# Kernel optimization log

Hardware: AMD Instinct MI355X
Metric: run time of the kernel (lower is better)

The kernel has to match this reference:

```python
import jax, jax.numpy as jnp
import numpy as np


def setup_inputs() -> dict:
    key = jax.random.key(0)
    ks = jax.random.split(key, 5)
    B, S, E, H = 2, 2048, 1024, 16
    scale = 1.0 / np.sqrt(E)
    return {
        "input": jax.random.normal(ks[0], (B, S, E), dtype=jnp.float32),
        "Wqkv": jax.random.normal(ks[1], (3 * E, E), dtype=jnp.float32) * scale,
        "bqkv": jax.random.normal(ks[2], (3 * E,), dtype=jnp.float32) * 0.01,
        "Wo": jax.random.normal(ks[3], (E, E), dtype=jnp.float32) * scale,
        "bo": jax.random.normal(ks[4], (E,), dtype=jnp.float32) * 0.01,
    }


def reference(input, Wqkv, bqkv, Wo, bo):
    H = 16
    B, S, E = input.shape
    dh = E // H
    # fused QKV projection: [B, S, 3E]
    qkv = input @ Wqkv.T + bqkv
    qkv = qkv.reshape(B, S, 3, H, dh)
    qkv = jnp.transpose(qkv, (2, 0, 3, 1, 4))  # [3, B, H, S, dh]
    q, k, v = qkv[0], qkv[1], qkv[2]
    # scores [B, H, Sq, Sk]
    scores = jnp.einsum("bhqd,bhkd->bhqk", q, k) / jnp.sqrt(jnp.float32(dh))
    # NOTE: original code softmaxes over dim=2 (the QUERY axis) — reproduced faithfully
    attn = jax.nn.softmax(scores, axis=2)
    out = jnp.einsum("bhqk,bhkd->bhqd", attn, v)  # [B, H, S, dh]
    out = jnp.transpose(out, (0, 2, 1, 3)).reshape(B, S, E)
    return out @ Wo.T + bo
```

## Files before the change

kernel.cpp:

```cpp
#include <hip/hip_runtime.h>
#include <math.h>

#define B_ 2
#define S_ 2048
#define E_ 1024
#define H_ 16
#define DH_ 64
#define NE3_ 3072
#define MTOT_ (B_*S_)
#define QSCALE_ 0.18033688011112042f

typedef __bf16 bf16;
typedef bf16 bf16x8 __attribute__((ext_vector_type(8)));
typedef bf16 bf16x4 __attribute__((ext_vector_type(4)));
typedef float f32x4 __attribute__((ext_vector_type(4)));
typedef float f32x16 __attribute__((ext_vector_type(16)));
typedef unsigned u32x2 __attribute__((ext_vector_type(2)));
typedef unsigned u32x4 __attribute__((ext_vector_type(4)));

#define MFMA16(a,b,c) __builtin_amdgcn_mfma_f32_16x16x32_bf16(a,b,c,0,0,0)
#define MFMA32(a,b,c) __builtin_amdgcn_mfma_f32_32x32x16_bf16(a,b,c,0,0,0)

#define F_(r) ((((r) & 7) ^ (((r) >> 3) & 7)))

__device__ inline void* lds_swz(void* base, int row, int bytecol) {
    return (char*)base + row * 128 + (bytecol ^ (F_(row) << 4));
}

__device__ inline unsigned cvt_pk_bf16(float lo, float hi) {
    unsigned r;
    asm("v_cvt_pk_bf16_f32 %0, %1, %2" : "=v"(r) : "v"(lo), "v"(hi));
    return r;
}

__device__ inline void permswap32(unsigned &x, unsigned &y) {
    u32x2 r = __builtin_amdgcn_permlane32_swap(x, y, false, false);
    x = r.x; y = r.y;
}

__device__ inline float exp2_hw(float x) {
    float r;
    asm("v_exp_f32 %0, %1" : "=v"(r) : "v"(x));
    return r;
}

__device__ inline void gload_lds16(const void* g, void* l) {
    __builtin_amdgcn_global_load_lds(
        (const __attribute__((address_space(1))) void*)g,
        (__attribute__((address_space(3))) void*)l, 16, 0, 0);
}

#define NX_ (MTOT_*E_)
#define NW_ (NE3_*E_)
#define NWO_ (E_*E_)
__global__ void k_f2b3(const float* __restrict__ x, const float* __restrict__ wq,
                       const float* __restrict__ wo,
                       bf16* __restrict__ xb, bf16* __restrict__ wqb,
                       bf16* __restrict__ wob) {
    const int i = blockIdx.x * 256 + threadIdx.x;
    const int idx = i * 4;
    const float* src; bf16* dst; int off;
    if (idx < NX_)            { src = x;  dst = xb;  off = idx; }
    else if (idx < NX_ + NW_) { src = wq; dst = wqb; off = idx - NX_; }
    else                      { src = wo; dst = wob; off = idx - NX_ - NW_; }
    float4 f = *reinterpret_cast<const float4*>(src + off);
    bf16x4 o;
    o[0] = (bf16)f.x; o[1] = (bf16)f.y; o[2] = (bf16)f.z; o[3] = (bf16)f.w;
    *reinterpret_cast<bf16x4*>(dst + off) = o;
}

template<int MODE>
__global__ __launch_bounds__(512) void k_gemm(
    const bf16* __restrict__ A, const bf16* __restrict__ W,
    const float* __restrict__ bias,
    bf16* __restrict__ Qf, bf16* __restrict__ Kf, bf16* __restrict__ Vf,
    float* __restrict__ out)
{
    constexpr int NBUF = (MODE == 0) ? 1 : 2;
    __shared__ __align__(16) bf16 At[NBUF][128*64];
    __shared__ __align__(16) bf16 Bt[NBUF][128*64];
    const int tid = threadIdx.x, lane = tid & 63, w = tid >> 6;
    const int lq = lane & 15, lh = lane >> 4;
    const int wr = w >> 2, wc = w & 3;
    const int g = blockIdx.x;
    const int nxw = (MODE == 0 ? 3 : 1);
    const int xcd = g & 7, li = g >> 3;
    const int m0 = (li & 31) * 128;
    const int n0 = (xcd * nxw + (li >> 5)) * 128;

    f32x4 acc[2][4] = {};

    auto stage = [&](int k0, int buf) {
        #pragma unroll
        for (int j = 0; j < 2; ++j) {
            const int idx = j*512 + tid;
            const int row = idx >> 3;
            const int colx = ((idx & 7) * 8) ^ (F_(row) * 8);
            gload_lds16(A + (size_t)(m0 + row) * E_ + k0 + colx, &At[buf][idx * 8]);
            gload_lds16(W + (size_t)(n0 + row) * E_ + k0 + colx, &Bt[buf][idx * 8]);
        }
    };
    auto compute = [&](int buf) {
        #pragma unroll
        for (int ks = 0; ks < 2; ++ks) {
            const int bc = ks * 64 + 16 * lh;
            bf16x8 a[4], b[2];
            #pragma unroll
            for (int j = 0; j < 4; ++j)
                a[j] = *(const bf16x8*)lds_swz(&At[buf][0], wr*64 + j*16 + lq, bc);
            #pragma unroll
            for (int i = 0; i < 2; ++i)
                b[i] = *(const bf16x8*)lds_swz(&Bt[buf][0], wc*32 + i*16 + lq, bc);
            #pragma unroll
            for (int i = 0; i < 2; ++i)
                #pragma unroll
                for (int j = 0; j < 4; ++j)
                    acc[i][j] = MFMA16(b[i], a[j], acc[i][j]);
        }
    };

    if constexpr (MODE == 0) {
        stage(0, 0);
        __syncthreads();
        for (int kt = 0; kt < E_/64; ++kt) {
            compute(0);
            if (kt + 1 < E_/64) {
                __syncthreads();
                stage((kt + 1) * 64, 0);
                __syncthreads();
            }
        }
    } else {
        stage(0, 0);
        __syncthreads();
        int cur = 0;
        for (int kt = 0; kt < E_/64; ++kt) {
            if (kt + 1 < E_/64) stage((kt + 1) * 64, cur ^ 1);
            compute(cur);
            cur ^= 1;
            if (kt + 1 < E_/64) __syncthreads();
        }
    }

    const int mW = m0 + wr*64;
    #pragma unroll
    for (int i = 0; i < 2; ++i) {
        const int n4 = n0 + wc*32 + i*16 + lh * 4;
        const float4 b4 = *reinterpret_cast<const float4*>(&bias[n4]);
        const float* bp = reinterpret_cast<const float*>(&b4);
        if constexpr (MODE == 0) {
            const int t = n4 >> 10, h = (n4 >> 6) & 15, d0 = n4 & 63;
            #pragma unroll
            for (int j = 0; j < 4; ++j) {
                const int m = mW + j*16 + lq;
                const int bb_i = m >> 11, s = m & 2047;
                const size_t bhb = ((size_t)(bb_i*H_ + h)) * 131072;
                if (t == 2) {
                    for (int r = 0; r < 4; ++r) {
                        const int d = d0 + r;
                        const size_t e = bhb + (size_t)(s >> 6) * 4096
                                       + ((d >> 5) * 4 + ((s >> 4) & 3)) * 512
                                       + ((d & 31) + 32 * ((s >> 3) & 1)) * 8
                                       + (s & 7);
                        Vf[e] = (bf16)(acc[i][j][r] + bp[r]);
                    }
                } else {
                    bf16* dst = (t == 0) ? Qf : Kf;
                    const float sc = (t == 0) ? QSCALE_ : 1.0f;
                    const size_t e = bhb + (size_t)(s >> 6) * 4096
                                   + (((s >> 5) & 1) * 4 + (d0 >> 4)) * 512
                                   + ((s & 31) + 32 * ((d0 >> 3) & 1)) * 8
                                   + (d0 & 7);
                    bf16x4 o;
                    for (int r = 0; r < 4; ++r)
                        o[r] = (bf16)((acc[i][j][r] + bp[r]) * sc);
                    *reinterpret_cast<bf16x4*>(dst + e) = o;
                }
            }
        } else {
            #pragma unroll
            for (int j = 0; j < 4; ++j) {
                const int m = mW + j*16 + lq;
                float4 o;
                o.x = acc[i][j][0] + bp[0];
                o.y = acc[i][j][1] + bp[1];
                o.z = acc[i][j][2] + bp[2];
                o.w = acc[i][j][3] + bp[3];
                *reinterpret_cast<float4*>(out + (size_t)m * E_ + n4) = o;
            }
        }
    }
}

__global__ __launch_bounds__(256) void k_colsum(
    const bf16* __restrict__ Qf, const bf16* __restrict__ Kf,
    bf16* __restrict__ Vf)
{
    __shared__ __align__(16) char smem[49152];
    __shared__ float rlbuf[128];
    char* Kl   = smem;
    char* Qbuf = smem + 16384;
    const int tid = threadIdx.x, lane = tid & 63, w = tid >> 6;
    const int l16 = lane * 16;
    const int g = blockIdx.x, xcd = g & 7, li = g >> 3;
    const int bh = xcd * 4 + (li >> 4);
    const int k0 = (li & 15) * 128;
    const bf16* Kbase = Kf + (size_t)bh * 131072 + (size_t)(k0 >> 6) * 4096;
    const bf16* Qbase = Qf + (size_t)bh * 131072;

    for (int j = 0; j < 4; ++j)
        gload_lds16(Kbase + (j*256 + tid)*8, Kl + (j*256 + w*64)*16);
    auto stageQ = [&](int qt, int buf) {
        const bf16* qb = Qbase + (size_t)qt * 8192;
        for (int j = 0; j < 4; ++j)
            gload_lds16(qb + (j*256 + tid)*8, Qbuf + buf*16384 + (j*256 + w*64)*16);
    };
    stageQ(0, 0);
    __syncthreads();

    bf16x8 bk[4];
    #pragma unroll
    for (int sl = 0; sl < 4; ++sl)
        bk[sl] = *(const bf16x8*)(Kl + w*4096 + sl*1024 + l16);

    float lsum = 0.f;
    int cur = 0;
    for (int qt = 0; qt < S_/128; ++qt) {
        if (qt + 1 < S_/128) stageQ(qt + 1, cur ^ 1);
        #pragma unroll
        for (int qs = 0; qs < 4; ++qs) {
            f32x16 s = {};
            __builtin_amdgcn_s_setprio(1);
            #pragma unroll
            for (int sl = 0; sl < 4; ++sl) {
                bf16x8 aq = *(const bf16x8*)(Qbuf + cur*16384 + (qs*4+sl)*1024 + l16);
                s = MFMA32(aq, bk[sl], s);
            }
            __builtin_amdgcn_s_setprio(0);
            #pragma unroll
            for (int r = 0; r < 16; ++r)
                lsum += exp2_hw(s[r]);
        }
        cur ^= 1;
        if (qt + 1 < S_/128) __syncthreads();
    }
    lsum += __shfl_xor(lsum, 32);
    if (lane < 32)
        rlbuf[w*32 + lane] = 1.0f / lsum;
    __syncthreads();

    bf16* Vb = Vf + (size_t)bh * 131072 + (size_t)(k0 >> 6) * 4096;
    for (int c = 0; c < 4; ++c) {
        const int v = c*256 + tid;
        const int kb = (v >> 9)*64 + ((v >> 6) & 3)*16 + ((v >> 5) & 1)*8;
        bf16x8* p = reinterpret_cast<bf16x8*>(Vb + v*8);
        bf16x8 x = *p, o;
        #pragma unroll
        for (int jj = 0; jj < 8; ++jj)
            o[jj] = (bf16)((float)x[jj] * rlbuf[kb + jj]);
        *p = o;
    }
}

__global__ __launch_bounds__(256) void k_attn(
    const bf16* __restrict__ Qf, const bf16* __restrict__ Kf,
    const bf16* __restrict__ Vf, bf16* __restrict__ AO)
{
    __shared__ __align__(16) char smem[49152];
    char* QP   = smem;
    char* Kbuf = smem + 16384;
    char* Vbuf = smem + 32768;
    const int tid = threadIdx.x, lane = tid & 63, w = tid >> 6;
    const int l16 = lane * 16;
    const int g = blockIdx.x, xcd = g & 7, li = g >> 3;
    const int bh = xcd * 4 + (li >> 4);
    const int q0 = (li & 15) * 128;
    const bf16* Qbase = Qf + (size_t)bh * 131072 + (size_t)(q0 >> 6) * 4096;
    const bf16* Kbase = Kf + (size_t)bh * 131072;
    const bf16* Vbase = Vf + (size_t)bh * 131072;

    for (int j = 0; j < 4; ++j)
        gload_lds16(Qbase + (j*256 + tid)*8, QP + (j*256 + w*64)*16);
    auto stageKV = [&](int kt, int buf) {
        const bf16* kb = Kbase + (size_t)kt * 4096;
        const bf16* vb = Vbase + (size_t)kt * 4096;
        for (int j = 0; j < 2; ++j) {
            gload_lds16(kb + (j*256 + tid)*8, Kbuf + buf*8192 + (j*256 + w*64)*16);
            gload_lds16(vb + (j*256 + tid)*8, Vbuf + buf*8192 + (j*256 + w*64)*16);
        }
    };
    stageKV(0, 0);
    __syncthreads();

    bf16x8 bq[4];
    #pragma unroll
    for (int sl = 0; sl < 4; ++sl)
        bq[sl] = *(const bf16x8*)(QP + w*4096 + sl*1024 + l16);

    f32x16 oacc[2] = {};
    int cur = 0;
    for (int t = 0; t < S_/64; ++t) {
        if (t + 1 < S_/64) stageKV(t + 1, cur ^ 1);
        char* Kc = Kbuf + cur*8192;
        char* Vc = Vbuf + cur*8192;

        #pragma unroll
        for (int kt = 0; kt < 2; ++kt) {
            f32x16 s = {};
            __builtin_amdgcn_s_setprio(1);
            #pragma unroll
            for (int sl = 0; sl < 4; ++sl) {
                bf16x8 ak = *(const bf16x8*)(Kc + (kt*4+sl)*1024 + l16);
                s = MFMA32(ak, bq[sl], s);
            }
            __builtin_amdgcn_s_setprio(0);

            unsigned a[8];
            #pragma unroll
            for (int gg = 0; gg < 8; ++gg)
                a[gg] = cvt_pk_bf16(exp2_hw(s[2*gg]), exp2_hw(s[2*gg+1]));

            #pragma unroll
            for (int kl = 0; kl < 2; ++kl) {
                unsigned m0 = a[4*kl + 0], m2 = a[4*kl + 2];
                unsigned m1 = a[4*kl + 1], m3 = a[4*kl + 3];
                permswap32(m0, m2);
                permswap32(m1, m3);
                u32x4 pw = {m0, m1, m2, m3};
                bf16x8 pf = __builtin_bit_cast(bf16x8, pw);
                const int ksl = kt*2 + kl;
                __builtin_amdgcn_s_setprio(1);
                #pragma unroll
                for (int dt = 0; dt < 2; ++dt) {
                    bf16x8 av = *(const bf16x8*)(Vc + (dt*4+ksl)*1024 + l16);
                    oacc[dt] = MFMA32(av, pf, oacc[dt]);
                }
                __builtin_amdgcn_s_setprio(0);
            }
        }
        cur ^= 1;
        if (t + 1 < S_/64) __syncthreads();
    }

    const int b = bh >> 4, h = bh & 15;
    const int q = q0 + w*32 + (lane & 31);
    const int hi4 = (lane >> 5) * 4;
    bf16* aob = AO + ((size_t)(b*S_ + q))*E_ + h*DH_;
    #pragma unroll
    for (int dt = 0; dt < 2; ++dt)
        #pragma unroll
        for (int rg = 0; rg < 4; ++rg) {
            const int dbase = dt*32 + 8*rg + hi4;
            bf16x4 o;
            #pragma unroll
            for (int r = 0; r < 4; ++r) o[r] = (bf16)oacc[dt][rg*4 + r];
            *reinterpret_cast<bf16x4*>(aob + dbase) = o;
        }
}

extern "C" void kernel_launch(void* const* d_in, const int* in_sizes, int n_in,
                              void* d_out, int out_size, void* d_ws, size_t ws_size,
                              hipStream_t stream) {
    const float* input = (const float*)d_in[0];
    const float* Wqkv  = (const float*)d_in[1];
    const float* bqkv  = (const float*)d_in[2];
    const float* Wo    = (const float*)d_in[3];
    const float* bo    = (const float*)d_in[4];
    float* out = (float*)d_out;

    char* ws = (char*)d_ws;
    bf16*  Xb   = (bf16*) (ws + 0);
    bf16*  Wqb  = (bf16*) (ws + 8388608);
    bf16*  Wob  = (bf16*) (ws + 14680064);
    bf16*  Qfg  = (bf16*) (ws + 16777216);
    bf16*  Kfg  = (bf16*) (ws + 25165824);
    bf16*  Vfg  = (bf16*) (ws + 33554432);
    bf16*  AO   = (bf16*) (ws + 41943040);

    k_f2b3<<<(NX_ + NW_ + NWO_) / 1024, 256, 0, stream>>>(
        input, Wqkv, Wo, Xb, Wqb, Wob);

    k_gemm<0><<<768, 512, 0, stream>>>(Xb, Wqb, bqkv, Qfg, Kfg, Vfg, nullptr);

    k_colsum<<<512, 256, 0, stream>>>(Qfg, Kfg, Vfg);

    k_attn<<<512, 256, 0, stream>>>(Qfg, Kfg, Vfg, AO);

    k_gemm<1><<<256, 512, 0, stream>>>(AO, Wob, bo, nullptr, nullptr, nullptr, out);
}
```

Before: 147.2 us.

## Load K/V fragments directly from global into registers, dropping LDS staging

The attention kernel no longer stages Q, K and V tiles through shared memory with barriers. Each wave now loads its MFMA operand fragments straight from global memory into registers, double-buffered across key tiles, and all __syncthreads are removed. This targets LDS round-trip and barrier costs, but every one of the four waves now fetches the same K/V data separately. That relies on L2/L1 to absorb the redundant traffic and raises register pressure from 32 extra bf16x8 registers.

```diff
diff --git a/kernel.cpp b/kernel.cpp
--- a/kernel.cpp
+++ b/kernel.cpp
@@ -266,53 +266,41 @@
     const bf16* __restrict__ Qf, const bf16* __restrict__ Kf,
     const bf16* __restrict__ Vf, bf16* __restrict__ AO)
 {
-    __shared__ __align__(16) char smem[49152];
-    char* QP   = smem;
-    char* Kbuf = smem + 16384;
-    char* Vbuf = smem + 32768;
     const int tid = threadIdx.x, lane = tid & 63, w = tid >> 6;
-    const int l16 = lane * 16;
     const int g = blockIdx.x, xcd = g & 7, li = g >> 3;
     const int bh = xcd * 4 + (li >> 4);
     const int q0 = (li & 15) * 128;
     const bf16* Qbase = Qf + (size_t)bh * 131072 + (size_t)(q0 >> 6) * 4096;
-    const bf16* Kbase = Kf + (size_t)bh * 131072;
-    const bf16* Vbase = Vf + (size_t)bh * 131072;
-
-    for (int j = 0; j < 4; ++j)
-        gload_lds16(Qbase + (j*256 + tid)*8, QP + (j*256 + w*64)*16);
-    auto stageKV = [&](int kt, int buf) {
-        const bf16* kb = Kbase + (size_t)kt * 4096;
-        const bf16* vb = Vbase + (size_t)kt * 4096;
-        for (int j = 0; j < 2; ++j) {
-            gload_lds16(kb + (j*256 + tid)*8, Kbuf + buf*8192 + (j*256 + w*64)*16);
-            gload_lds16(vb + (j*256 + tid)*8, Vbuf + buf*8192 + (j*256 + w*64)*16);
-        }
-    };
-    stageKV(0, 0);
-    __syncthreads();
+    const bf16* Kbase = Kf + (size_t)bh * 131072 + (size_t)lane * 8;
+    const bf16* Vbase = Vf + (size_t)bh * 131072 + (size_t)lane * 8;
 
     bf16x8 bq[4];
     #pragma unroll
     for (int sl = 0; sl < 4; ++sl)
-        bq[sl] = *(const bf16x8*)(QP + w*4096 + sl*1024 + l16);
+        bq[sl] = *(const bf16x8*)(Qbase + (w >> 1)*4096 + ((w & 1)*4 + sl)*512
+                                  + (size_t)lane*8);
+
+    bf16x8 kf0[8], kf1[8], vf0[8], vf1[8];
+    auto loadKV = [&](int t, bf16x8 (&kd)[8], bf16x8 (&vd)[8]) {
+        const bf16* kb = Kbase + (size_t)t * 4096;
+        const bf16* vb = Vbase + (size_t)t * 4096;
+        #pragma unroll
+        for (int c = 0; c < 8; ++c) {
+            kd[c] = *(const bf16x8*)(kb + c*512);
+            vd[c] = *(const bf16x8*)(vb + c*512);
+        }
+    };
 
     f32x16 oacc[2] = {};
-    int cur = 0;
-    for (int t = 0; t < S_/64; ++t) {
-        if (t + 1 < S_/64) stageKV(t + 1, cur ^ 1);
-        char* Kc = Kbuf + cur*8192;
-        char* Vc = Vbuf + cur*8192;
-
+
+    auto compute = [&](bf16x8 (&kd)[8], bf16x8 (&vd)[8]) {
         #pragma unroll
         for (int kt = 0; kt < 2; ++kt) {
             f32x16 s = {};
             __builtin_amdgcn_s_setprio(1);
             #pragma unroll
-            for (int sl = 0; sl < 4; ++sl) {
-                bf16x8 ak = *(const bf16x8*)(Kc + (kt*4+sl)*1024 + l16);
-                s = MFMA32(ak, bq[sl], s);
-            }
+            for (int sl = 0; sl < 4; ++sl)
+                s = MFMA32(kd[kt*4 + sl], bq[sl], s);
             __builtin_amdgcn_s_setprio(0);
 
             unsigned a[8];
@@ -331,15 +319,19 @@
                 const int ksl = kt*2 + kl;
                 __builtin_amdgcn_s_setprio(1);
                 #pragma unroll
-                for (int dt = 0; dt < 2; ++dt) {
-                    bf16x8 av = *(const bf16x8*)(Vc + (dt*4+ksl)*1024 + l16);
-                    oacc[dt] = MFMA32(av, pf, oacc[dt]);
-                }
+                for (int dt = 0; dt < 2; ++dt)
+                    oacc[dt] = MFMA32(vd[dt*4 + ksl], pf, oacc[dt]);
                 __builtin_amdgcn_s_setprio(0);
             }
         }
-        cur ^= 1;
-        if (t + 1 < S_/64) __syncthreads();
+    };
+
+    loadKV(0, kf0, vf0);
+    for (int t = 0; t < 32; t += 2) {
+        if (t + 1 < 32) loadKV(t + 1, kf1, vf1);
+        compute(kf0, vf0);
+        if (t + 2 < 32) loadKV(t + 2, kf0, vf0);
+        if (t + 1 < 32) compute(kf1, vf1);
     }
 
     const int b = bh >> 4, h = bh & 15;
```

Measured after the change: 152.2 us. +3.4%, slower.
